# Kernel tuning notes

Measured on AMD Instinct MI355X. Metric: run time of the kernel, lower is better.

The kernel has to match this reference:

```python
import jax, jax.numpy as jnp
import numpy as np

D_MODEL = 1024

def setup_inputs() -> dict:
    key = jax.random.key(0)
    ks = jax.random.split(key, 8)
    B, S, D = 8, 2048, D_MODEL
    scale = 1.0 / np.sqrt(D)
    return {
        "x1": jax.random.normal(ks[0], (B, S, D), dtype=jnp.float32),
        "x2": jax.random.normal(ks[1], (B, S, D), dtype=jnp.float32),
        "Wq": jax.random.normal(ks[2], (D, D), dtype=jnp.float32) * scale,
        "bq": jnp.zeros((D,), dtype=jnp.float32),
        "Wk": jax.random.normal(ks[3], (D, D), dtype=jnp.float32) * scale,
        "bk": jnp.zeros((D,), dtype=jnp.float32),
        "Wv": jax.random.normal(ks[4], (D, D), dtype=jnp.float32) * scale,
        "bv": jnp.zeros((D,), dtype=jnp.float32),
    }

def reference(x1, x2, Wq, bq, Wk, bk, Wv, bv):
    # q1: [B, Sq, D]; k2, v2: [B, Sk, D]
    q1 = jnp.einsum('bsd,de->bse', x1, Wq) + bq
    k2 = jnp.einsum('bsd,de->bse', x2, Wk) + bk
    v2 = jnp.einsum('bsd,de->bse', x2, Wv) + bv
    scale = 1.0 / np.sqrt(q1.shape[-1]).astype(np.float32)
    scores = jnp.einsum('bqd,bkd->bqk', q1, k2) * scale  # [B, Sq, Sk]
    probs = jax.nn.softmax(scores, axis=-1)
    return jnp.einsum('bqk,bkd->bqd', probs, v2)
```

## Files before the change

### kernel.cpp

```cpp
#include <hip/hip_runtime.h>
#include <hip/hip_bf16.h>
#include <hip/hip_fp16.h>

typedef __attribute__((ext_vector_type(8))) short short8;
typedef __attribute__((ext_vector_type(4))) float f32x4;

#define DEVI __device__ __forceinline__

DEVI unsigned short f2bf(float f){
  __hip_bfloat16 h = __float2bfloat16(f);
  unsigned short u; __builtin_memcpy(&u, &h, 2); return u;
}

__global__ void cast_f32_bf16(const float* __restrict__ in, unsigned short* __restrict__ out, int n4){
  int stride = gridDim.x * blockDim.x;
  for (int i = blockIdx.x*blockDim.x + threadIdx.x; i < n4; i += stride){
    float4 f = reinterpret_cast<const float4*>(in)[i];
    ushort4 o;
    o.x = f2bf(f.x); o.y = f2bf(f.y); o.z = f2bf(f.z); o.w = f2bf(f.w);
    reinterpret_cast<ushort4*>(out)[i] = o;
  }
}

__global__ void transpose_cast_w(const float* __restrict__ W, unsigned short* __restrict__ WT, int K, int N){
  __shared__ float tile[32][33];
  int bn = blockIdx.x*32, bk = blockIdx.y*32;
  int tx = threadIdx.x & 31, ty = threadIdx.x >> 5;
  for (int r=0;r<32;r+=8)
    tile[ty+r][tx] = W[(long)(bk+ty+r)*N + bn+tx];
  __syncthreads();
  for (int r=0;r<32;r+=8)
    WT[(long)(bn+ty+r)*K + bk+tx] = (short)f2bf(tile[tx][ty+r]);
}

DEVI void stage16(const short* gsrc, short* lbase){
  __builtin_amdgcn_global_load_lds(
      (const __attribute__((address_space(1))) unsigned int*)gsrc,
      (__attribute__((address_space(3))) unsigned int*)lbase, 16, 0, 0);
}

DEVI void stage2(const short* base, long o0, long o1, short* blk, int w){
  stage16(base + o0, blk + w*512);
  stage16(base + o1, blk + (8+w)*512);
}

template<int OT, int BIAS>
__global__ __launch_bounds__(512, 2)
void gemm8(const short* __restrict__ A, const short* __restrict__ Bt,
           const float* __restrict__ bias, void* __restrict__ Cv,
           int N, int K, long sA, long sB, long sC, float scale, int nx, int ny)
{
  extern __shared__ short lds[];
  const int nwg = gridDim.x;
  const int cpx = nwg >> 3;
  const int wg  = (blockIdx.x & 7)*cpx + (blockIdx.x >> 3);
  const int bx  = wg % nx;
  const int tmp = wg / nx;
  const int by  = tmp % ny;
  const long bz = tmp / ny;
  const int m0 = bx * 256, n0 = by * 256;
  const short* Ab = A  + bz*sA + (long)m0 * K;
  const short* Bb = Bt + bz*sB + (long)n0 * K;

  const int t = threadIdx.x, lane = t & 63, w = t >> 6;
  const int wr = w >> 2, wc = w & 3;

  const int rr = lane >> 2;
  const int kk = ((lane & 3) * 8) ^ ((lane & 32) ? 16 : 0);
  const long off0 = (long)(( w     )*16 + rr) * K + kk;
  const long off1 = (long)(( 8 + w )*16 + rr) * K + kk;

  const int la = lane & 15;
  const int lsw = (la*64 + ((lane>>4)<<4)) ^ ((la>=8)?32:0);
  const short* AP = lds + (lsw>>1) + wr*4096;
  const short* BP = lds + (lsw>>1) + 16384 + wc*2048;

  f32x4 acc[8][4] = {};

  const int NT = K >> 6;
  const int niter = NT >> 1;

  stage2(Ab,      off0, off1, lds + 0,     w);
  stage2(Bb,      off0, off1, lds + 16384, w);
  stage2(Ab + 32, off0, off1, lds + 8192,  w);
  stage2(Bb + 32, off0, off1, lds + 24576, w);
  stage2(Ab + 64, off0, off1, lds + 32768, w);
  stage2(Bb + 64, off0, off1, lds + 49152, w);
  asm volatile("s_waitcnt vmcnt(4)" ::: "memory");
  asm volatile("s_barrier" ::: "memory");

#define MFMA4(MI, AV)                                                           \
    acc[MI][0] = __builtin_amdgcn_mfma_f32_16x16x32_bf16(AV, b0_, acc[MI][0], 0,0,0); \
    acc[MI][1] = __builtin_amdgcn_mfma_f32_16x16x32_bf16(AV, b1_, acc[MI][1], 0,0,0); \
    acc[MI][2] = __builtin_amdgcn_mfma_f32_16x16x32_bf16(AV, b2_, acc[MI][2], 0,0,0); \
    acc[MI][3] = __builtin_amdgcn_mfma_f32_16x16x32_bf16(AV, b3_, acc[MI][3], 0,0,0);

#define PHPAIR(CBUF, QK, SB0, SO0, SL0, SB1, SO1, SL1, TAILVM) do {             \
    const short* bp_ = BP + (CBUF)*32768 + (QK)*8192;                           \
    short8 b0_ = *reinterpret_cast<const short8*>(bp_ + 0*512);                 \
    short8 b1_ = *reinterpret_cast<const short8*>(bp_ + 1*512);                 \
    short8 b2_ = *reinterpret_cast<const short8*>(bp_ + 2*512);                 \
    short8 b3_ = *reinterpret_cast<const short8*>(bp_ + 3*512);                 \
    const short* ap_ = AP + (CBUF)*32768 + (QK)*8192;                           \
    short8 a0_ = *reinterpret_cast<const short8*>(ap_ + 0*512);                 \
    short8 a1_ = *reinterpret_cast<const short8*>(ap_ + 1*512);                 \
    short8 a2_ = *reinterpret_cast<const short8*>(ap_ + 2*512);                 \
    short8 a3_ = *reinterpret_cast<const short8*>(ap_ + 3*512);                 \
    short8 a4_ = *reinterpret_cast<const short8*>(ap_ + 2048 + 0*512);          \
    short8 a5_ = *reinterpret_cast<const short8*>(ap_ + 2048 + 1*512);          \
    short8 a6_ = *reinterpret_cast<const short8*>(ap_ + 2048 + 2*512);          \
    short8 a7_ = *reinterpret_cast<const short8*>(ap_ + 2048 + 3*512);          \
    stage2((SB0) + (SO0), off0, off1, lds + (SL0), w);                          \
    asm volatile("s_waitcnt lgkmcnt(4)" ::: "memory");                          \
    __builtin_amdgcn_sched_barrier(0);                                          \
    __builtin_amdgcn_s_setprio(1);                                              \
    MFMA4(0, a0_) MFMA4(1, a1_) MFMA4(2, a2_) MFMA4(3, a3_)                     \
    __builtin_amdgcn_s_setprio(0);                                              \
    __builtin_amdgcn_sched_barrier(0);                                          \
    asm volatile("s_barrier" ::: "memory");                                     \
    stage2((SB1) + (SO1), off0, off1, lds + (SL1), w);                          \
    asm volatile("s_waitcnt lgkmcnt(0)" ::: "memory");                          \
    __builtin_amdgcn_sched_barrier(0);                                          \
    __builtin_amdgcn_s_setprio(1);                                              \
    MFMA4(4, a4_) MFMA4(5, a5_) MFMA4(6, a6_) MFMA4(7, a7_)                     \
    __builtin_amdgcn_s_setprio(0);                                              \
    __builtin_amdgcn_sched_barrier(0);                                          \
    if (TAILVM) asm volatile("s_waitcnt vmcnt(4)" ::: "memory");                \
    asm volatile("s_barrier" ::: "memory");                                     \
  } while(0)

  for (int it = 0; it < niter; ++it){
    const int u  = it*2;
    int u1 = u+1; if (u1 >= NT) u1 -= NT;
    int u2 = u+2; if (u2 >= NT) u2 -= NT;
    int u3 = u+3; if (u3 >= NT) u3 -= NT;
    const int k1 = u1*64, k2 = u2*64, k3 = u3*64;
    PHPAIR(0, 0, Ab, k1+32, 40960, Bb, k1+32, 57344, 0);
    PHPAIR(0, 1, Ab, k2,    0,     Bb, k2,    16384, 1);
    PHPAIR(1, 0, Ab, k2+32, 8192,  Bb, k2+32, 24576, 0);
    PHPAIR(1, 1, Ab, k3,    32768, Bb, k3,    49152, 1);
  }
#undef PHPAIR
#undef MFMA4

  asm volatile("s_waitcnt vmcnt(0) lgkmcnt(0)" ::: "memory");
  __syncthreads();

  {
    char* sb = (char*)lds;
    constexpr int STRB = (OT==0) ? 1056 : 544;
    const int tr = t >> 4, tcE = (t & 15) * 16;
    const int grow = m0 + (tr>>4)*128 + (tr&15);
    #pragma unroll
    for (int mi = 0; mi < 8; ++mi){
      __syncthreads();
      #pragma unroll
      for (int nj = 0; nj < 4; ++nj){
        const int c = wc*64 + la + nj*16;
        float badd = (BIAS==1) ? bias[n0 + c] : 0.0f;
        #pragma unroll
        for (int j = 0; j < 4; ++j){
          const int lr = wr*16 + ((lane>>4)<<2) + j;
          float v = acc[mi][nj][j] * scale + badd;
          if (BIAS==2) v += bias[m0 + (lr>>4)*128 + mi*16 + (lr&15)];
          if constexpr (OT==0){
            const int byte = lr*STRB + ((((c>>2) ^ (lr&15)))<<4) + (c&3)*4;
            *reinterpret_cast<float*>(sb + byte) = v;
          } else if constexpr (OT==1){
            const int byte = lr*STRB + ((((c>>3) ^ (lr&15)))<<4) + (c&7)*2;
            *reinterpret_cast<__half*>(sb + byte) = __float2half(v);
          } else {
            const int byte = lr*STRB + ((((c>>3) ^ (lr&15)))<<4) + (c&7)*2;
            *reinterpret_cast<unsigned short*>(sb + byte) = f2bf(v);
          }
        }
      }
      __syncthreads();
      const long gbase = bz*sC + (long)(grow + mi*16)*N + n0 + tcE;
      if constexpr (OT==0){
        const int cb = tcE >> 2;
        #pragma unroll
        for (int i=0;i<4;i++){
          f32x4 vv = *reinterpret_cast<const f32x4*>(sb + tr*STRB + (((cb+i)^(tr&15))<<4));
          *reinterpret_cast<f32x4*>((float*)Cv + gbase + i*4) = vv;
        }
      } else {
        const int cb = tcE >> 3;
        #pragma unroll
        for (int i=0;i<2;i++){
          short8 vv = *reinterpret_cast<const short8*>(sb + tr*STRB + (((cb+i)^(tr&15))<<4));
          *reinterpret_cast<short8*>((unsigned short*)Cv + gbase + i*8) = vv;
        }
      }
    }
  }
}

__global__ void softmax_rows(unsigned short* __restrict__ SP, int cols){
  const long row = blockIdx.x;
  unsigned short* rp = SP + row * cols;
  const int t = threadIdx.x, lane = t & 63, w = t >> 6;
  short8 raw = *reinterpret_cast<const short8*>(rp + t*8);
  float v[8];
  #pragma unroll
  for (int i=0;i<8;i++){
    unsigned short us = (unsigned short)raw[i];
    __half h; __builtin_memcpy(&h, &us, 2);
    v[i] = __half2float(h);
  }
  float m = v[0];
  #pragma unroll
  for (int i=1;i<8;i++) m = fmaxf(m, v[i]);
  #pragma unroll
  for (int o=32;o;o>>=1) m = fmaxf(m, __shfl_down(m, o));
  __shared__ float red[8];
  if (lane==0) red[w] = m;
  __syncthreads();
  if (t==0) red[4] = fmaxf(fmaxf(red[0],red[1]), fmaxf(red[2],red[3]));
  __syncthreads();
  const float rowmax = red[4];
  float s = 0.f;
  #pragma unroll
  for (int i=0;i<8;i++){ v[i] = __expf(v[i]-rowmax); s += v[i]; }
  #pragma unroll
  for (int o=32;o;o>>=1) s += __shfl_down(s, o);
  if (lane==0) red[w] = s;
  __syncthreads();
  if (t==0) red[5] = red[0]+red[1]+red[2]+red[3];
  __syncthreads();
  const float inv = 1.0f / red[5];
  short8 outp;
  #pragma unroll
  for (int i=0;i<8;i++) outp[i] = (short)f2bf(v[i]*inv);
  *reinterpret_cast<short8*>(rp + t*8) = outp;
}

extern "C" void kernel_launch(void* const* d_in, const int* in_sizes, int n_in,
                              void* d_out, int out_size, void* d_ws, size_t ws_size,
                              hipStream_t stream)
{
  const int B = 8, S = 2048, D = 1024;
  const int BS = B * S;
  const float* x1 = (const float*)d_in[0];
  const float* x2 = (const float*)d_in[1];
  const float* Wq = (const float*)d_in[2];
  const float* bq = (const float*)d_in[3];
  const float* Wk = (const float*)d_in[4];
  const float* bk = (const float*)d_in[5];
  const float* Wv = (const float*)d_in[6];
  const float* bv = (const float*)d_in[7];

  char* ws = (char*)d_ws;
  const size_t MB = 1024*1024;
  short*          x1b = (short*)(ws);
  short*          x2b = (short*)(ws + 32*MB);
  unsigned short* Sc  = (unsigned short*)ws;
  short*          q   = (short*)(ws + 64*MB);
  short*          k   = (short*)(ws + 96*MB);
  short*          vT  = (short*)(ws + 128*MB);
  short*          WqT = (short*)(ws + 160*MB);
  short*          WkT = (short*)(ws + 162*MB);
  short*          WvT = (short*)(ws + 164*MB);

  const size_t SH = 131072;

  cast_f32_bf16<<<4096,256,0,stream>>>(x1, (unsigned short*)x1b, BS*D/4);
  cast_f32_bf16<<<4096,256,0,stream>>>(x2, (unsigned short*)x2b, BS*D/4);
  transpose_cast_w<<<dim3(32,32),256,0,stream>>>(Wq, (unsigned short*)WqT, D, D);
  transpose_cast_w<<<dim3(32,32),256,0,stream>>>(Wk, (unsigned short*)WkT, D, D);
  transpose_cast_w<<<dim3(32,32),256,0,stream>>>(Wv, (unsigned short*)WvT, D, D);

  gemm8<2,1><<<256, 512, SH, stream>>>(x2b, WkT, bk, k, D, D, 0,0,0, 1.0f, 64, 4);
  gemm8<2,2><<<256, 512, SH, stream>>>(WvT, x2b, bv, vT, S, D, 0, (long)S*D, (long)D*S, 1.0f, 4, 8);
  gemm8<2,1><<<256, 512, SH, stream>>>(x1b, WqT, bq, q, D, D, 0,0,0, 1.0f, 64, 4);
  gemm8<1,0><<<512, 512, SH, stream>>>(q, k, nullptr, Sc, S, D,
                                       (long)S*D, (long)S*D, (long)S*S, 0.03125f, 8, 8);
  softmax_rows<<<BS,256,0,stream>>>(Sc, S);
  gemm8<0,0><<<256, 512, SH, stream>>>((short*)Sc, vT, nullptr, d_out, D, S,
                                       (long)S*S, (long)D*S, (long)S*D, 1.0f, 8, 4);
}
```

Measured before the change: 342.7 us.

## Software-pipeline LDS fragment reads across phases with double-buffered registers

```diff
diff --git a/kernel.cpp b/kernel.cpp
--- a/kernel.cpp
+++ b/kernel.cpp
@@ -89,43 +89,49 @@
   asm volatile("s_waitcnt vmcnt(4)" ::: "memory");
   asm volatile("s_barrier" ::: "memory");
 
-#define MFMA4(MI, AV)                                                           \
-    acc[MI][0] = __builtin_amdgcn_mfma_f32_16x16x32_bf16(AV, b0_, acc[MI][0], 0,0,0); \
-    acc[MI][1] = __builtin_amdgcn_mfma_f32_16x16x32_bf16(AV, b1_, acc[MI][1], 0,0,0); \
-    acc[MI][2] = __builtin_amdgcn_mfma_f32_16x16x32_bf16(AV, b2_, acc[MI][2], 0,0,0); \
-    acc[MI][3] = __builtin_amdgcn_mfma_f32_16x16x32_bf16(AV, b3_, acc[MI][3], 0,0,0);
-
-#define PHPAIR(CBUF, QK, SB0, SO0, SL0, SB1, SO1, SL1, TAILVM) do {             \
-    const short* bp_ = BP + (CBUF)*32768 + (QK)*8192;                           \
-    short8 b0_ = *reinterpret_cast<const short8*>(bp_ + 0*512);                 \
-    short8 b1_ = *reinterpret_cast<const short8*>(bp_ + 1*512);                 \
-    short8 b2_ = *reinterpret_cast<const short8*>(bp_ + 2*512);                 \
-    short8 b3_ = *reinterpret_cast<const short8*>(bp_ + 3*512);                 \
-    const short* ap_ = AP + (CBUF)*32768 + (QK)*8192;                           \
-    short8 a0_ = *reinterpret_cast<const short8*>(ap_ + 0*512);                 \
-    short8 a1_ = *reinterpret_cast<const short8*>(ap_ + 1*512);                 \
-    short8 a2_ = *reinterpret_cast<const short8*>(ap_ + 2*512);                 \
-    short8 a3_ = *reinterpret_cast<const short8*>(ap_ + 3*512);                 \
-    short8 a4_ = *reinterpret_cast<const short8*>(ap_ + 2048 + 0*512);          \
-    short8 a5_ = *reinterpret_cast<const short8*>(ap_ + 2048 + 1*512);          \
-    short8 a6_ = *reinterpret_cast<const short8*>(ap_ + 2048 + 2*512);          \
-    short8 a7_ = *reinterpret_cast<const short8*>(ap_ + 2048 + 3*512);          \
-    stage2((SB0) + (SO0), off0, off1, lds + (SL0), w);                          \
+  short8 Bx0,Bx1,Bx2,Bx3, A0x0,A0x1,A0x2,A0x3;
+  short8 By0,By1,By2,By3, A0y0,A0y1,A0y2,A0y3;
+  short8 A10,A11,A12,A13;
+
+#define RD4(d0,d1,d2,d3, P) \
+    d0 = *reinterpret_cast<const short8*>((P) + 0*512); \
+    d1 = *reinterpret_cast<const short8*>((P) + 1*512); \
+    d2 = *reinterpret_cast<const short8*>((P) + 2*512); \
+    d3 = *reinterpret_cast<const short8*>((P) + 3*512);
+
+  RD4(Bx0,Bx1,Bx2,Bx3, BP)
+  RD4(A0x0,A0x1,A0x2,A0x3, AP)
+
+#define MM4(MI, AV, C0,C1,C2,C3) \
+    acc[MI][0] = __builtin_amdgcn_mfma_f32_16x16x32_bf16(AV, C0, acc[MI][0], 0,0,0); \
+    acc[MI][1] = __builtin_amdgcn_mfma_f32_16x16x32_bf16(AV, C1, acc[MI][1], 0,0,0); \
+    acc[MI][2] = __builtin_amdgcn_mfma_f32_16x16x32_bf16(AV, C2, acc[MI][2], 0,0,0); \
+    acc[MI][3] = __builtin_amdgcn_mfma_f32_16x16x32_bf16(AV, C3, acc[MI][3], 0,0,0);
+
+#define PH_A(B0,B1,B2,B3, Q0,Q1,Q2,Q3, CBUF, QK, SBASE, SOFF, SL) do {          \
+    const short* a1p_ = AP + (CBUF)*32768 + (QK)*8192 + 2048;                   \
+    RD4(A10,A11,A12,A13, a1p_)                                                  \
+    stage2((SBASE) + (SOFF), off0, off1, lds + (SL), w);                        \
     asm volatile("s_waitcnt lgkmcnt(4)" ::: "memory");                          \
-    __builtin_amdgcn_sched_barrier(0);                                          \
     __builtin_amdgcn_s_setprio(1);                                              \
-    MFMA4(0, a0_) MFMA4(1, a1_) MFMA4(2, a2_) MFMA4(3, a3_)                     \
+    MM4(0, Q0, B0,B1,B2,B3) MM4(1, Q1, B0,B1,B2,B3)                             \
+    MM4(2, Q2, B0,B1,B2,B3) MM4(3, Q3, B0,B1,B2,B3)                             \
     __builtin_amdgcn_s_setprio(0);                                              \
-    __builtin_amdgcn_sched_barrier(0);                                          \
     asm volatile("s_barrier" ::: "memory");                                     \
-    stage2((SB1) + (SO1), off0, off1, lds + (SL1), w);                          \
-    asm volatile("s_waitcnt lgkmcnt(0)" ::: "memory");                          \
-    __builtin_amdgcn_sched_barrier(0);                                          \
+  } while(0)
+
+#define PH_B(B0,B1,B2,B3, N0,N1,N2,N3, P0,P1,P2,P3, NCBUF, NQK, SBASE, SOFF, SL) do { \
+    const short* bp_ = BP + (NCBUF)*32768 + (NQK)*8192;                         \
+    const short* ap_ = AP + (NCBUF)*32768 + (NQK)*8192;                         \
+    RD4(N0,N1,N2,N3, bp_)                                                       \
+    RD4(P0,P1,P2,P3, ap_)                                                       \
+    stage2((SBASE) + (SOFF), off0, off1, lds + (SL), w);                        \
+    asm volatile("s_waitcnt lgkmcnt(8)" ::: "memory");                          \
     __builtin_amdgcn_s_setprio(1);                                              \
-    MFMA4(4, a4_) MFMA4(5, a5_) MFMA4(6, a6_) MFMA4(7, a7_)                     \
+    MM4(4, A10, B0,B1,B2,B3) MM4(5, A11, B0,B1,B2,B3)                           \
+    MM4(6, A12, B0,B1,B2,B3) MM4(7, A13, B0,B1,B2,B3)                           \
     __builtin_amdgcn_s_setprio(0);                                              \
-    __builtin_amdgcn_sched_barrier(0);                                          \
-    if (TAILVM) asm volatile("s_waitcnt vmcnt(4)" ::: "memory");                \
+    asm volatile("s_waitcnt vmcnt(4)" ::: "memory");                            \
     asm volatile("s_barrier" ::: "memory");                                     \
   } while(0)
 
@@ -135,13 +141,23 @@
     int u2 = u+2; if (u2 >= NT) u2 -= NT;
     int u3 = u+3; if (u3 >= NT) u3 -= NT;
     const int k1 = u1*64, k2 = u2*64, k3 = u3*64;
-    PHPAIR(0, 0, Ab, k1+32, 40960, Bb, k1+32, 57344, 0);
-    PHPAIR(0, 1, Ab, k2,    0,     Bb, k2,    16384, 1);
-    PHPAIR(1, 0, Ab, k2+32, 8192,  Bb, k2+32, 24576, 0);
-    PHPAIR(1, 1, Ab, k3,    32768, Bb, k3,    49152, 1);
-  }
-#undef PHPAIR
-#undef MFMA4
+    PH_A(Bx0,Bx1,Bx2,Bx3, A0x0,A0x1,A0x2,A0x3, 0,0, Ab, k1+32, 40960);
+    PH_B(Bx0,Bx1,Bx2,Bx3, By0,By1,By2,By3, A0y0,A0y1,A0y2,A0y3, 0,1,
+         Bb, k1+32, 57344);
+    PH_A(By0,By1,By2,By3, A0y0,A0y1,A0y2,A0y3, 0,1, Ab, k2, 0);
+    PH_B(By0,By1,By2,By3, Bx0,Bx1,Bx2,Bx3, A0x0,A0x1,A0x2,A0x3, 1,0,
+         Bb, k2, 16384);
+    PH_A(Bx0,Bx1,Bx2,Bx3, A0x0,A0x1,A0x2,A0x3, 1,0, Ab, k2+32, 8192);
+    PH_B(Bx0,Bx1,Bx2,Bx3, By0,By1,By2,By3, A0y0,A0y1,A0y2,A0y3, 1,1,
+         Bb, k2+32, 24576);
+    PH_A(By0,By1,By2,By3, A0y0,A0y1,A0y2,A0y3, 1,1, Ab, k3, 32768);
+    PH_B(By0,By1,By2,By3, Bx0,Bx1,Bx2,Bx3, A0x0,A0x1,A0x2,A0x3, 0,0,
+         Bb, k3, 49152);
+  }
+#undef PH_A
+#undef PH_B
+#undef MM4
+#undef RD4
 
   asm volatile("s_waitcnt vmcnt(0) lgkmcnt(0)" ::: "memory");
   __syncthreads();
```

Result: no change. 340.9 us (-0.5%).
